# Optimization experiments

Measured on AMD Instinct MI355X. Metric: run time of the kernel, lower is better.

The kernel has to match this reference:

```python
import jax, jax.numpy as jnp
import numpy as np

IDIM = 1024
HIDDEN = 4096
N_EXPERT = 8
T = 2048


def setup_inputs() -> dict:
    key = jax.random.key(0)
    ks = jax.random.split(key, 6)
    s_in = 1.0 / np.sqrt(IDIM)
    s_h = 1.0 / np.sqrt(HIDDEN)
    return {
        "xs": jax.random.normal(ks[0], (T, IDIM), dtype=jnp.float32),
        "top_k": 2,
        # gate: Linear(idim -> n_expert, bias=False); torch weight (E, D)
        "Wg": jax.random.uniform(ks[1], (N_EXPERT, IDIM), jnp.float32, -s_in, s_in),
        # experts stacked: w_1 Linear(idim->hidden), w_2 Linear(hidden->idim)
        "W1": jax.random.uniform(ks[2], (N_EXPERT, IDIM, HIDDEN), jnp.float32, -s_in, s_in),
        "b1": jax.random.uniform(ks[3], (N_EXPERT, HIDDEN), jnp.float32, -s_in, s_in),
        "W2": jax.random.uniform(ks[4], (N_EXPERT, HIDDEN, IDIM), jnp.float32, -s_h, s_h),
        "b2": jax.random.uniform(ks[5], (N_EXPERT, IDIM), jnp.float32, -s_h, s_h),
    }


def reference(xs, top_k, Wg, W1, b1, W2, b2):
    # Router: (T, E)
    router = xs @ Wg.T
    logits, selected = jax.lax.top_k(router, top_k)          # (T, k)
    # softmax over the top-k slot axis in fp32, cast back (matches torch)
    weights = jax.nn.softmax(logits.astype(jnp.float32), axis=-1).astype(xs.dtype)
    # combine weight per token per expert: (T, E). Tokens not routed to an
    # expert get weight 0, zeroing that expert's contribution (same math as
    # the masked gather / scatter-add in the torch loop).
    onehot = jax.nn.one_hot(selected, N_EXPERT, dtype=xs.dtype)  # (T, k, E)
    comb = jnp.einsum("tk,tke->te", weights, onehot)
    # all-expert FFN (dropout_rate = 0 -> identity)
    h = jax.nn.relu(jnp.einsum("td,edh->teh", xs, W1) + b1[None, :, :])
    y = jnp.einsum("teh,ehd->ted", h, W2) + b2[None, :, :]
    return jnp.einsum("te,ted->td", comb, y)
```

## Files before the change

### kernel.cpp

```cpp
#include <hip/hip_runtime.h>
#include <stdint.h>

#define T_TOK 2048
#define IDIM  1024
#define HID   4096
#define NE    8
#define BM    128
#define BN    128
#define BN2   64
#define BK    64
#define RMAX  5120
#define MAXTILES 40

typedef __bf16 bf16;
typedef bf16  bf16x8 __attribute__((ext_vector_type(8)));
typedef float f32x4  __attribute__((ext_vector_type(4)));

#define WS_NTILES   128
#define WS_TILE_E   192
#define WS_TILE_R   448
#define WS_TOK_E    1024
#define WS_TOK_W    17408
#define WS_ROW_TOK  33792
#define WS_ROW_W    54272
#define WS_TOK_POS  74752
#define XG_OFF      131072

__device__ __forceinline__ int xcd_remap(int orig, int nwg) {
    int q = nwg >> 3, r = nwg & 7;
    int xcd = orig & 7, idx = orig >> 3;
    return (xcd < r ? xcd * (q + 1) : r * (q + 1) + (xcd - r) * q) + idx;
}

__global__ __launch_bounds__(256) void k_router(const float* __restrict__ xs,
                                                const float* __restrict__ Wg,
                                                int* __restrict__ tok_e,
                                                float* __restrict__ tok_w) {
    __shared__ float sWg[NE * IDIM];
    for (int i = threadIdx.x; i < NE * IDIM; i += 256) sWg[i] = Wg[i];
    __syncthreads();
    int wave = threadIdx.x >> 6, lane = threadIdx.x & 63;
    int t = blockIdx.x * 4 + wave;
    if (t >= T_TOK) return;
    float p[NE];
#pragma unroll
    for (int e = 0; e < NE; e++) p[e] = 0.f;
    for (int j = 0; j < IDIM / 64; j++) {
        float x = xs[(size_t)t * IDIM + j * 64 + lane];
#pragma unroll
        for (int e = 0; e < NE; e++)
            p[e] += x * sWg[e * IDIM + j * 64 + lane];
    }
#pragma unroll
    for (int e = 0; e < NE; e++) {
        float v = p[e];
        for (int off = 32; off > 0; off >>= 1) v += __shfl_down(v, off);
        p[e] = v;
    }
    if (lane == 0) {
        int e0 = 0; float l0 = p[0];
        for (int e = 1; e < NE; e++) if (p[e] > l0) { l0 = p[e]; e0 = e; }
        int e1 = -1; float l1 = -1e30f;
        for (int e = 0; e < NE; e++) if (e != e0 && p[e] > l1) { l1 = p[e]; e1 = e; }
        if (e1 < 0) e1 = (e0 + 1) & 7;
        float z = __expf(l1 - l0);
        tok_e[2 * t]     = e0;  tok_e[2 * t + 1] = e1;
        tok_w[2 * t]     = 1.f / (1.f + z);
        tok_w[2 * t + 1] = z / (1.f + z);
    }
}

__global__ __launch_bounds__(256) void k_setup(int* __restrict__ w,
                                               float* __restrict__ wf) {
    __shared__ int cnt[NE];
    __shared__ int cur[NE];
    int tid = threadIdx.x;
    if (tid < NE) cnt[tid] = 0;
    for (int i = tid; i < RMAX; i += 256) w[WS_ROW_TOK / 4 + i] = -1;
    __syncthreads();
    for (int i = tid; i < 2 * T_TOK; i += 256)
        atomicAdd(&cnt[w[WS_TOK_E / 4 + i]], 1);
    __syncthreads();
    if (tid == 0) {
        int off = 0, nt = 0;
        for (int e = 0; e < NE; e++) {
            cur[e] = off;
            int nb = (cnt[e] + BM - 1) / BM;
            for (int b = 0; b < nb && nt < MAXTILES; b++) {
                w[WS_TILE_E / 4 + nt] = e;
                w[WS_TILE_R / 4 + nt] = off + b * BM;
                nt++;
            }
            off += nb * BM;
        }
        w[WS_NTILES / 4] = nt;
    }
    __syncthreads();
    for (int i = tid; i < 2 * T_TOK; i += 256) {
        int e   = w[WS_TOK_E / 4 + i];
        int pos = atomicAdd(&cur[e], 1);
        if (pos < RMAX) {
            w[WS_ROW_TOK / 4 + pos] = i >> 1;
            wf[WS_ROW_W / 4 + pos]  = wf[WS_TOK_W / 4 + i];
            w[WS_TOK_POS / 4 + i]   = pos;
        } else {
            w[WS_TOK_POS / 4 + i]   = 0;
        }
    }
}

__device__ inline uint4 pack8(float4 a, float4 b) {
    union { bf16 h[8]; uint4 u; } pk;
    pk.h[0] = (bf16)a.x; pk.h[1] = (bf16)a.y; pk.h[2] = (bf16)a.z; pk.h[3] = (bf16)a.w;
    pk.h[4] = (bf16)b.x; pk.h[5] = (bf16)b.y; pk.h[6] = (bf16)b.z; pk.h[7] = (bf16)b.w;
    return pk.u;
}
__device__ inline uint32_t pack2(float a, float b) {
    union { bf16 h[2]; uint32_t u; } pk;
    pk.h[0] = (bf16)a; pk.h[1] = (bf16)b;
    return pk.u;
}

__device__ __forceinline__ void g2l16(const bf16* g, bf16* l) {
    __builtin_amdgcn_global_load_lds(
        (const __attribute__((address_space(1))) void*)g,
        (__attribute__((address_space(3))) void*)l, 16, 0, 0);
}

__global__ __launch_bounds__(256) void k_gather(const float* __restrict__ xs,
                                                const int* __restrict__ wsi,
                                                bf16* __restrict__ Xg) {
    int wv = threadIdx.x >> 6, lane = threadIdx.x & 63;
    int r = blockIdx.x * 4 + wv;
    int tok = wsi[WS_ROW_TOK / 4 + r];
#pragma unroll
    for (int i = 0; i < 2; i++) {
        int c = i * 64 + lane;
        uint4 v;
        if (tok >= 0) {
            const float* g = xs + (size_t)tok * IDIM + c * 8;
            v = pack8(*(const float4*)g, *(const float4*)(g + 4));
        } else v = make_uint4(0u, 0u, 0u, 0u);
        int cs = (c & ~7) | ((c & 7) ^ (r & 7));
        *(uint4*)&Xg[(size_t)r * IDIM + cs * 8] = v;
    }
}

__global__ __launch_bounds__(256) void k_cvt(const float* __restrict__ src,
                                             bf16* __restrict__ dst,
                                             int ld_src, int k0, int n0, int KL,
                                             size_t s_estride, size_t d_estride) {
    __shared__ bf16 sT[64 * 66];
    int e = blockIdx.y;
    const float* S = src + (size_t)e * s_estride;
    bf16* D = dst + (size_t)e * d_estride;
    int ntk = KL >> 6;
    int tk = blockIdx.x % ntk, tn = blockIdx.x / ntk;
    int t = threadIdx.x;
#pragma unroll
    for (int i = 0; i < 4; i++) {
        int idx = t + i * 256;
        int k = idx >> 4, n4 = (idx & 15) * 4;
        float4 v = *(const float4*)&S[(size_t)(k0 + tk * 64 + k) * ld_src +
                                      n0 + tn * 64 + n4];
        *(uint32_t*)&sT[k * 66 + n4]     = pack2(v.x, v.y);
        *(uint32_t*)&sT[k * 66 + n4 + 2] = pack2(v.z, v.w);
    }
    __syncthreads();
#pragma unroll
    for (int j = 0; j < 2; j++) {
        int idx = t + j * 256;
        int n = idx >> 3, kq = idx & 7;
        union { bf16 h[8]; uint4 u; } pk;
#pragma unroll
        for (int jj = 0; jj < 8; jj++) pk.h[jj] = sT[(kq * 8 + jj) * 66 + n];
        int ng = tn * 64 + n;
        int ch = kq ^ (ng & 7);
        *(uint4*)&D[(size_t)ng * KL + tk * 64 + ch * 8] = pk.u;
    }
}

__global__ __launch_bounds__(256) void k_ffn1n(const bf16* __restrict__ Xg,
                                               const bf16* __restrict__ W1t,
                                               const float* __restrict__ b1,
                                               const int* __restrict__ wsi,
                                               bf16* __restrict__ H,
                                               int h0, int CW) {
    int gx = gridDim.x;
    int orig = blockIdx.x + gx * blockIdx.y;
    int wgid = xcd_remap(orig, gx * gridDim.y);
    int bx = wgid % gx, tile = wgid / gx;
    if (tile >= wsi[WS_NTILES / 4]) return;
    int e    = wsi[WS_TILE_E / 4 + tile];
    int row0 = wsi[WS_TILE_R / 4 + tile];
    int n0   = bx * BN;

    const bf16* Abase = Xg + (size_t)row0 * IDIM;
    const bf16* Bbase = W1t + ((size_t)e * CW + n0) * IDIM;

    __shared__ bf16 sA[BM * BK];
    __shared__ bf16 sB[BN * BK];

    int t = threadIdx.x, lane = t & 63;
    int wv = t >> 6, wx = wv & 1, wy = wv >> 1;
    int lm = lane & 15, q = lane >> 4;

    f32x4 acc[4][4];
#pragma unroll
    for (int i = 0; i < 4; i++)
#pragma unroll
        for (int j = 0; j < 4; j++) acc[i][j] = (f32x4){0.f, 0.f, 0.f, 0.f};

    for (int kc = 0; kc < IDIM / BK; kc++) {
        if (kc) __syncthreads();
#pragma unroll
        for (int i = 0; i < 4; i++) {
            int s = t + i * 256;
            g2l16(Abase + (size_t)(s >> 3) * IDIM + kc * BK + (s & 7) * 8,
                  &sA[s * 8]);
        }
#pragma unroll
        for (int i = 0; i < 4; i++) {
            int s = t + i * 256;
            g2l16(Bbase + (size_t)(s >> 3) * IDIM + kc * BK + (s & 7) * 8,
                  &sB[s * 8]);
        }
        __syncthreads();
#pragma unroll
        for (int ks = 0; ks < 2; ks++) {
            bf16x8 aF[4], bF[4];
#pragma unroll
            for (int mt = 0; mt < 4; mt++) {
                int r = wy * 64 + mt * 16 + lm;
                aF[mt] = *(const bf16x8*)&sA[r * BK + (((ks * 4 + q) ^ (r & 7)) * 8)];
            }
#pragma unroll
            for (int nt = 0; nt < 4; nt++) {
                int r = wx * 64 + nt * 16 + lm;
                bF[nt] = *(const bf16x8*)&sB[r * BK + (((ks * 4 + q) ^ (r & 7)) * 8)];
            }
#pragma unroll
            for (int mt = 0; mt < 4; mt++)
#pragma unroll
                for (int nt = 0; nt < 4; nt++)
                    acc[mt][nt] = __builtin_amdgcn_mfma_f32_16x16x32_bf16(
                        aF[mt], bF[nt], acc[mt][nt], 0, 0, 0);
        }
    }
#pragma unroll
    for (int nt = 0; nt < 4; nt++) {
        int col = n0 + wx * 64 + nt * 16 + lm;
        float bv = b1[(size_t)e * HID + h0 + col];
#pragma unroll
        for (int mt = 0; mt < 4; mt++) {
#pragma unroll
            for (int r = 0; r < 4; r++) {
                int rg = row0 + wy * 64 + mt * 16 + q * 4 + r;
                float v = fmaxf(acc[mt][nt][r] + bv, 0.f);
                int sc = (col & ~63) | ((col & 63) ^ ((rg & 7) << 3));
                H[(size_t)rg * CW + sc] = (bf16)v;
            }
        }
    }
}

__global__ __launch_bounds__(256) void k_ffn2y(const bf16* __restrict__ H,
                                               const bf16* __restrict__ W2t,
                                               const float* __restrict__ b2,
                                               const int* __restrict__ wsi,
                                               float* __restrict__ Y,
                                               int CW, int first) {
    int gx = gridDim.x;
    int orig = blockIdx.x + gx * blockIdx.y;
    int wgid = xcd_remap(orig, gx * gridDim.y);
    int bx = wgid % gx, tile = wgid / gx;
    if (tile >= wsi[WS_NTILES / 4]) return;
    int e    = wsi[WS_TILE_E / 4 + tile];
    int row0 = wsi[WS_TILE_R / 4 + tile];
    int n0   = bx * BN2;

    const bf16* Abase = H + (size_t)row0 * CW;
    const bf16* Bbase = W2t + ((size_t)e * IDIM + n0) * CW;

    __shared__ bf16 sA[BM * BK];
    __shared__ bf16 sB[BN2 * BK];

    int t = threadIdx.x, lane = t & 63;
    int wv = t >> 6, wx = wv & 1, wy = wv >> 1;
    int lm = lane & 15, q = lane >> 4;

    f32x4 acc[4][2];
#pragma unroll
    for (int i = 0; i < 4; i++)
#pragma unroll
        for (int j = 0; j < 2; j++) acc[i][j] = (f32x4){0.f, 0.f, 0.f, 0.f};

    for (int kc = 0; kc < CW / BK; kc++) {
        if (kc) __syncthreads();
#pragma unroll
        for (int i = 0; i < 4; i++) {
            int s = t + i * 256;
            g2l16(Abase + (size_t)(s >> 3) * CW + kc * BK + (s & 7) * 8,
                  &sA[s * 8]);
        }
#pragma unroll
        for (int i = 0; i < 2; i++) {
            int s = t + i * 256;
            g2l16(Bbase + (size_t)(s >> 3) * CW + kc * BK + (s & 7) * 8,
                  &sB[s * 8]);
        }
        __syncthreads();
#pragma unroll
        for (int ks = 0; ks < 2; ks++) {
            bf16x8 aF[4], bF[2];
#pragma unroll
            for (int mt = 0; mt < 4; mt++) {
                int r = wy * 64 + mt * 16 + lm;
                aF[mt] = *(const bf16x8*)&sA[r * BK + (((ks * 4 + q) ^ (r & 7)) * 8)];
            }
#pragma unroll
            for (int nt = 0; nt < 2; nt++) {
                int r = wx * 32 + nt * 16 + lm;
                bF[nt] = *(const bf16x8*)&sB[r * BK + (((ks * 4 + q) ^ (r & 7)) * 8)];
            }
#pragma unroll
            for (int mt = 0; mt < 4; mt++)
#pragma unroll
                for (int nt = 0; nt < 2; nt++)
                    acc[mt][nt] = __builtin_amdgcn_mfma_f32_16x16x32_bf16(
                        aF[mt], bF[nt], acc[mt][nt], 0, 0, 0);
        }
    }

#pragma unroll
    for (int nt = 0; nt < 2; nt++) {
        int col  = n0 + wx * 32 + nt * 16 + lm;
        float bv = first ? b2[(size_t)e * IDIM + col] : 0.f;
#pragma unroll
        for (int mt = 0; mt < 4; mt++)
#pragma unroll
            for (int r = 0; r < 4; r++) {
                int rg = row0 + wy * 64 + mt * 16 + q * 4 + r;
                float* p = &Y[(size_t)rg * IDIM + col];
                float v  = acc[mt][nt][r] + bv;
                *p = first ? v : (*p + v);
            }
    }
}

__global__ __launch_bounds__(256) void k_combine(const float* __restrict__ Y,
                                                 const int* __restrict__ wsi,
                                                 const float* __restrict__ wsf,
                                                 float* __restrict__ out) {
    int tok = blockIdx.x;
    int p0 = wsi[WS_TOK_POS / 4 + 2 * tok];
    int p1 = wsi[WS_TOK_POS / 4 + 2 * tok + 1];
    float w0 = wsf[WS_TOK_W / 4 + 2 * tok];
    float w1 = wsf[WS_TOK_W / 4 + 2 * tok + 1];
    int c = threadIdx.x;
    const float4* y0 = (const float4*)(Y + (size_t)p0 * IDIM);
    const float4* y1 = (const float4*)(Y + (size_t)p1 * IDIM);
    float4 a = y0[c], b = y1[c];
    float4 r;
    r.x = w0 * a.x + w1 * b.x;
    r.y = w0 * a.y + w1 * b.y;
    r.z = w0 * a.z + w1 * b.z;
    r.w = w0 * a.w + w1 * b.w;
    ((float4*)(out + (size_t)tok * IDIM))[c] = r;
}

__global__ __launch_bounds__(256) void k_fallback(const float* __restrict__ xs,
                                                  const float* __restrict__ Wg,
                                                  const float* __restrict__ W1,
                                                  const float* __restrict__ b1,
                                                  const float* __restrict__ W2,
                                                  const float* __restrict__ b2,
                                                  float* __restrict__ out) {
    __shared__ float xbuf[IDIM];
    __shared__ float hbuf[256];
    __shared__ float slog[NE];
    __shared__ int   sel[2];
    __shared__ float selw[2];

    int t   = blockIdx.x;
    int tid = threadIdx.x;

    for (int i = tid; i < IDIM; i += 256)
        xbuf[i] = xs[(size_t)t * IDIM + i];
    __syncthreads();
    {
        int e = tid >> 5, l = tid & 31;
        float p = 0.f;
        for (int d = l; d < IDIM; d += 32)
            p += xbuf[d] * Wg[e * IDIM + d];
        for (int off = 16; off > 0; off >>= 1) p += __shfl_down(p, off, 32);
        if (l == 0) slog[e] = p;
    }
    __syncthreads();
    if (tid == 0) {
        int e0 = 0; float l0 = slog[0];
        for (int e = 1; e < NE; e++) if (slog[e] > l0) { l0 = slog[e]; e0 = e; }
        int e1 = -1; float l1 = -1e30f;
        for (int e = 0; e < NE; e++) if (e != e0 && slog[e] > l1) { l1 = slog[e]; e1 = e; }
        if (e1 < 0) e1 = (e0 + 1) & 7;
        float z = __expf(l1 - l0);
        sel[0] = e0; sel[1] = e1;
        selw[0] = 1.f / (1.f + z);
        selw[1] = z / (1.f + z);
    }
    __syncthreads();

    float ytot[4] = {0.f, 0.f, 0.f, 0.f};
#pragma unroll
    for (int s = 0; s < 2; s++) {
        int   e = sel[s];
        float w = selw[s];
        const float* W1e = W1 + (size_t)e * IDIM * HID;
        const float* W2e = W2 + (size_t)e * HID * IDIM;
        float ys[4] = {0.f, 0.f, 0.f, 0.f};
        for (int hb = 0; hb < HID / 256; hb++) {
            int h = hb * 256 + tid;
            float acc = b1[e * HID + h];
            for (int d = 0; d < IDIM; d++)
                acc += xbuf[d] * W1e[(size_t)d * HID + h];
            __syncthreads();
            hbuf[tid] = fmaxf(acc, 0.f);
            __syncthreads();
            for (int hh = 0; hh < 256; hh++) {
                float hv = hbuf[hh];
                const float* wrow = W2e + (size_t)(hb * 256 + hh) * IDIM;
#pragma unroll
                for (int cc = 0; cc < 4; cc++)
                    ys[cc] += hv * wrow[cc * 256 + tid];
            }
        }
#pragma unroll
        for (int cc = 0; cc < 4; cc++)
            ytot[cc] += w * (ys[cc] + b2[e * IDIM + cc * 256 + tid]);
    }
#pragma unroll
    for (int cc = 0; cc < 4; cc++)
        out[(size_t)t * IDIM + cc * 256 + tid] = ytot[cc];
}

extern "C" void kernel_launch(void* const* d_in, const int* in_sizes, int n_in,
                              void* d_out, int out_size, void* d_ws, size_t ws_size,
                              hipStream_t stream) {
    int o = (n_in >= 7 && in_sizes[1] == 1) ? 1 : 0;
    const float* xs = (const float*)d_in[0];
    const float* Wg = (const float*)d_in[1 + o];
    const float* W1 = (const float*)d_in[2 + o];
    const float* b1 = (const float*)d_in[3 + o];
    const float* W2 = (const float*)d_in[4 + o];
    const float* b2 = (const float*)d_in[5 + o];
    float* out = (float*)d_out;

    size_t xg_sz = (size_t)RMAX * IDIM * 2;
    size_t y_sz  = (size_t)RMAX * IDIM * 4;
    int CW = 0;
    if (d_ws) {
        for (int c = HID; c >= 512; c >>= 1) {
            size_t need = (size_t)XG_OFF + xg_sz + (size_t)RMAX * c * 2 +
                          (size_t)NE * c * IDIM * 2 + y_sz;
            if (ws_size >= need) { CW = c; break; }
        }
    }
    if (!CW) {
        k_fallback<<<T_TOK, 256, 0, stream>>>(xs, Wg, W1, b1, W2, b2, out);
        return;
    }

    char*  ws  = (char*)d_ws;
    int*   wsi = (int*)d_ws;
    float* wsf = (float*)d_ws;
    bf16*  Xg  = (bf16*)(ws + XG_OFF);
    bf16*  Hb  = (bf16*)(ws + XG_OFF + xg_sz);
    bf16*  Wt  = (bf16*)(ws + XG_OFF + xg_sz + (size_t)RMAX * CW * 2);
    float* Yb  = (float*)(ws + XG_OFF + xg_sz + (size_t)RMAX * CW * 2 +
                          (size_t)NE * CW * IDIM * 2);

    k_router<<<T_TOK / 4, 256, 0, stream>>>(xs, Wg, wsi + WS_TOK_E / 4,
                                            wsf + WS_TOK_W / 4);
    k_setup<<<1, 256, 0, stream>>>(wsi, wsf);
    k_gather<<<RMAX / 4, 256, 0, stream>>>(xs, wsi, Xg);

    int HC = HID / CW;
    for (int c = 0; c < HC; c++) {
        k_cvt<<<dim3((IDIM / 64) * (CW / 64), NE), 256, 0, stream>>>(
            W1, Wt, HID, 0, c * CW, IDIM,
            (size_t)IDIM * HID, (size_t)CW * IDIM);
        k_ffn1n<<<dim3(CW / BN, MAXTILES), 256, 0, stream>>>(
            Xg, Wt, b1, wsi, Hb, c * CW, CW);
        k_cvt<<<dim3((CW / 64) * (IDIM / 64), NE), 256, 0, stream>>>(
            W2, Wt, IDIM, c * CW, 0, CW,
            (size_t)HID * IDIM, (size_t)IDIM * CW);
        k_ffn2y<<<dim3(IDIM / BN2, MAXTILES), 256, 0, stream>>>(
            Hb, Wt, b2, wsi, Yb, CW, c == 0 ? 1 : 0);
    }
    k_combine<<<T_TOK, 256, 0, stream>>>(Yb, wsi, wsf, out);
}
```

Before: 438.5 us.

## Double-buffer LDS in FFN GEMMs, stage H stores, batch cvt tiles per block

```diff
diff --git a/kernel.cpp b/kernel.cpp
--- a/kernel.cpp
+++ b/kernel.cpp
@@ -149,34 +149,39 @@
 __global__ __launch_bounds__(256) void k_cvt(const float* __restrict__ src,
                                              bf16* __restrict__ dst,
                                              int ld_src, int k0, int n0, int KL,
-                                             size_t s_estride, size_t d_estride) {
+                                             size_t s_estride, size_t d_estride,
+                                             int tpb) {
     __shared__ bf16 sT[64 * 66];
-    int e = blockIdx.y;
+    int e = blockIdx.z;
     const float* S = src + (size_t)e * s_estride;
     bf16* D = dst + (size_t)e * d_estride;
-    int ntk = KL >> 6;
-    int tk = blockIdx.x % ntk, tn = blockIdx.x / ntk;
+    int tn  = blockIdx.x;
+    int tk0 = blockIdx.y * tpb;
     int t = threadIdx.x;
-#pragma unroll
-    for (int i = 0; i < 4; i++) {
-        int idx = t + i * 256;
-        int k = idx >> 4, n4 = (idx & 15) * 4;
-        float4 v = *(const float4*)&S[(size_t)(k0 + tk * 64 + k) * ld_src +
-                                      n0 + tn * 64 + n4];
-        *(uint32_t*)&sT[k * 66 + n4]     = pack2(v.x, v.y);
-        *(uint32_t*)&sT[k * 66 + n4 + 2] = pack2(v.z, v.w);
-    }
-    __syncthreads();
-#pragma unroll
-    for (int j = 0; j < 2; j++) {
-        int idx = t + j * 256;
-        int n = idx >> 3, kq = idx & 7;
-        union { bf16 h[8]; uint4 u; } pk;
-#pragma unroll
-        for (int jj = 0; jj < 8; jj++) pk.h[jj] = sT[(kq * 8 + jj) * 66 + n];
-        int ng = tn * 64 + n;
-        int ch = kq ^ (ng & 7);
-        *(uint4*)&D[(size_t)ng * KL + tk * 64 + ch * 8] = pk.u;
+    for (int tt = 0; tt < tpb; tt++) {
+        int tk = tk0 + tt;
+        if (tt) __syncthreads();
+#pragma unroll
+        for (int i = 0; i < 4; i++) {
+            int idx = t + i * 256;
+            int k = idx >> 4, n4 = (idx & 15) * 4;
+            float4 v = *(const float4*)&S[(size_t)(k0 + tk * 64 + k) * ld_src +
+                                          n0 + tn * 64 + n4];
+            *(uint32_t*)&sT[k * 66 + n4]     = pack2(v.x, v.y);
+            *(uint32_t*)&sT[k * 66 + n4 + 2] = pack2(v.z, v.w);
+        }
+        __syncthreads();
+#pragma unroll
+        for (int j = 0; j < 2; j++) {
+            int idx = t + j * 256;
+            int n = idx >> 3, kq = idx & 7;
+            union { bf16 h[8]; uint4 u; } pk;
+#pragma unroll
+            for (int jj = 0; jj < 8; jj++) pk.h[jj] = sT[(kq * 8 + jj) * 66 + n];
+            int ng = tn * 64 + n;
+            int ch = kq ^ (ng & 7);
+            *(uint4*)&D[(size_t)ng * KL + tk * 64 + ch * 8] = pk.u;
+        }
     }
 }
 
@@ -198,8 +203,8 @@
     const bf16* Abase = Xg + (size_t)row0 * IDIM;
     const bf16* Bbase = W1t + ((size_t)e * CW + n0) * IDIM;
 
-    __shared__ bf16 sA[BM * BK];
-    __shared__ bf16 sB[BN * BK];
+    __shared__ bf16 sA[2][BM * BK];
+    __shared__ bf16 sB[2][BN * BK];
 
     int t = threadIdx.x, lane = t & 63;
     int wv = t >> 6, wx = wv & 1, wy = wv >> 1;
@@ -211,33 +216,40 @@
 #pragma unroll
         for (int j = 0; j < 4; j++) acc[i][j] = (f32x4){0.f, 0.f, 0.f, 0.f};
 
-    for (int kc = 0; kc < IDIM / BK; kc++) {
-        if (kc) __syncthreads();
+    auto stage = [&](int kc, int b) {
 #pragma unroll
         for (int i = 0; i < 4; i++) {
             int s = t + i * 256;
             g2l16(Abase + (size_t)(s >> 3) * IDIM + kc * BK + (s & 7) * 8,
-                  &sA[s * 8]);
+                  &sA[b][s * 8]);
         }
 #pragma unroll
         for (int i = 0; i < 4; i++) {
             int s = t + i * 256;
             g2l16(Bbase + (size_t)(s >> 3) * IDIM + kc * BK + (s & 7) * 8,
-                  &sB[s * 8]);
-        }
-        __syncthreads();
+                  &sB[b][s * 8]);
+        }
+    };
+
+    stage(0, 0);
+    __syncthreads();
+    for (int kc = 0; kc < IDIM / BK; kc++) {
+        int cur = kc & 1;
+        if (kc + 1 < IDIM / BK) stage(kc + 1, cur ^ 1);
+        const bf16* A = sA[cur];
+        const bf16* B = sB[cur];
 #pragma unroll
         for (int ks = 0; ks < 2; ks++) {
             bf16x8 aF[4], bF[4];
 #pragma unroll
             for (int mt = 0; mt < 4; mt++) {
                 int r = wy * 64 + mt * 16 + lm;
-                aF[mt] = *(const bf16x8*)&sA[r * BK + (((ks * 4 + q) ^ (r & 7)) * 8)];
+                aF[mt] = *(const bf16x8*)&A[r * BK + (((ks * 4 + q) ^ (r & 7)) * 8)];
             }
 #pragma unroll
             for (int nt = 0; nt < 4; nt++) {
                 int r = wx * 64 + nt * 16 + lm;
-                bF[nt] = *(const bf16x8*)&sB[r * BK + (((ks * 4 + q) ^ (r & 7)) * 8)];
+                bF[nt] = *(const bf16x8*)&B[r * BK + (((ks * 4 + q) ^ (r & 7)) * 8)];
             }
 #pragma unroll
             for (int mt = 0; mt < 4; mt++)
@@ -246,21 +258,33 @@
                     acc[mt][nt] = __builtin_amdgcn_mfma_f32_16x16x32_bf16(
                         aF[mt], bF[nt], acc[mt][nt], 0, 0, 0);
         }
-    }
+        __syncthreads();
+    }
+
+    bf16* sC = &sA[0][0];
 #pragma unroll
     for (int nt = 0; nt < 4; nt++) {
-        int col = n0 + wx * 64 + nt * 16 + lm;
-        float bv = b1[(size_t)e * HID + h0 + col];
+        int col_l = wx * 64 + nt * 16 + lm;
+        float bv  = b1[(size_t)e * HID + h0 + n0 + col_l];
 #pragma unroll
         for (int mt = 0; mt < 4; mt++) {
 #pragma unroll
             for (int r = 0; r < 4; r++) {
-                int rg = row0 + wy * 64 + mt * 16 + q * 4 + r;
+                int rloc = wy * 64 + mt * 16 + q * 4 + r;
+                int rg   = row0 + rloc;
                 float v = fmaxf(acc[mt][nt][r] + bv, 0.f);
-                int sc = (col & ~63) | ((col & 63) ^ ((rg & 7) << 3));
-                H[(size_t)rg * CW + sc] = (bf16)v;
-            }
-        }
+                int sc = (col_l & ~63) | ((col_l & 63) ^ ((rg & 7) << 3));
+                sC[rloc * BN + sc] = (bf16)v;
+            }
+        }
+    }
+    __syncthreads();
+#pragma unroll
+    for (int i = 0; i < 8; i++) {
+        int u = t + i * 256;
+        int row = u >> 4, c = u & 15;
+        uint4 v = *(const uint4*)&sC[row * BN + c * 8];
+        *(uint4*)&H[(size_t)(row0 + row) * CW + n0 + c * 8] = v;
     }
 }
 
@@ -282,8 +306,8 @@
     const bf16* Abase = H + (size_t)row0 * CW;
     const bf16* Bbase = W2t + ((size_t)e * IDIM + n0) * CW;
 
-    __shared__ bf16 sA[BM * BK];
-    __shared__ bf16 sB[BN2 * BK];
+    __shared__ bf16 sA[2][BM * BK];
+    __shared__ bf16 sB[2][BN2 * BK];
 
     int t = threadIdx.x, lane = t & 63;
     int wv = t >> 6, wx = wv & 1, wy = wv >> 1;
@@ -295,33 +319,41 @@
 #pragma unroll
         for (int j = 0; j < 2; j++) acc[i][j] = (f32x4){0.f, 0.f, 0.f, 0.f};
 
-    for (int kc = 0; kc < CW / BK; kc++) {
-        if (kc) __syncthreads();
+    auto stage = [&](int kc, int b) {
 #pragma unroll
         for (int i = 0; i < 4; i++) {
             int s = t + i * 256;
             g2l16(Abase + (size_t)(s >> 3) * CW + kc * BK + (s & 7) * 8,
-                  &sA[s * 8]);
+                  &sA[b][s * 8]);
         }
 #pragma unroll
         for (int i = 0; i < 2; i++) {
             int s = t + i * 256;
             g2l16(Bbase + (size_t)(s >> 3) * CW + kc * BK + (s & 7) * 8,
-                  &sB[s * 8]);
-        }
-        __syncthreads();
+                  &sB[b][s * 8]);
+        }
+    };
+
+    int kiters = CW / BK;
+    stage(0, 0);
+    __syncthreads();
+    for (int kc = 0; kc < kiters; kc++) {
+        int cur = kc & 1;
+        if (kc + 1 < kiters) stage(kc + 1, cur ^ 1);
+        const bf16* A = sA[cur];
+        const bf16* B = sB[cur];
 #pragma unroll
         for (int ks = 0; ks < 2; ks++) {
             bf16x8 aF[4], bF[2];
 #pragma unroll
             for (int mt = 0; mt < 4; mt++) {
                 int r = wy * 64 + mt * 16 + lm;
-                aF[mt] = *(const bf16x8*)&sA[r * BK + (((ks * 4 + q) ^ (r & 7)) * 8)];
+                aF[mt] = *(const bf16x8*)&A[r * BK + (((ks * 4 + q) ^ (r & 7)) * 8)];
             }
 #pragma unroll
             for (int nt = 0; nt < 2; nt++) {
                 int r = wx * 32 + nt * 16 + lm;
-                bF[nt] = *(const bf16x8*)&sB[r * BK + (((ks * 4 + q) ^ (r & 7)) * 8)];
+                bF[nt] = *(const bf16x8*)&B[r * BK + (((ks * 4 + q) ^ (r & 7)) * 8)];
             }
 #pragma unroll
             for (int mt = 0; mt < 4; mt++)
@@ -330,6 +362,7 @@
                     acc[mt][nt] = __builtin_amdgcn_mfma_f32_16x16x32_bf16(
                         aF[mt], bF[nt], acc[mt][nt], 0, 0, 0);
         }
+        __syncthreads();
     }
 
 #pragma unroll
@@ -486,14 +519,24 @@
 
     int HC = HID / CW;
     for (int c = 0; c < HC; c++) {
-        k_cvt<<<dim3((IDIM / 64) * (CW / 64), NE), 256, 0, stream>>>(
-            W1, Wt, HID, 0, c * CW, IDIM,
-            (size_t)IDIM * HID, (size_t)CW * IDIM);
+        {
+            int ntn = CW / 64, ntk = IDIM / 64;
+            int tpb = ntk;
+            while (ntn * NE * (ntk / tpb) < 1024 && tpb > 1) tpb >>= 1;
+            k_cvt<<<dim3(ntn, ntk / tpb, NE), 256, 0, stream>>>(
+                W1, Wt, HID, 0, c * CW, IDIM,
+                (size_t)IDIM * HID, (size_t)CW * IDIM, tpb);
+        }
         k_ffn1n<<<dim3(CW / BN, MAXTILES), 256, 0, stream>>>(
             Xg, Wt, b1, wsi, Hb, c * CW, CW);
-        k_cvt<<<dim3((CW / 64) * (IDIM / 64), NE), 256, 0, stream>>>(
-            W2, Wt, IDIM, c * CW, 0, CW,
-            (size_t)HID * IDIM, (size_t)IDIM * CW);
+        {
+            int ntn = IDIM / 64, ntk = CW / 64;
+            int tpb = ntk;
+            while (ntn * NE * (ntk / tpb) < 1024 && tpb > 1) tpb >>= 1;
+            k_cvt<<<dim3(ntn, ntk / tpb, NE), 256, 0, stream>>>(
+                W2, Wt, IDIM, c * CW, 0, CW,
+                (size_t)HID * IDIM, (size_t)IDIM * CW, tpb);
+        }
         k_ffn2y<<<dim3(IDIM / BN2, MAXTILES), 256, 0, stream>>>(
             Hb, Wt, b2, wsi, Yb, CW, c == 0 ? 1 : 0);
     }
```

Measured after the change: 455.8 us. +3.9%, slower.
